# Performance work log

Measured on AMD Instinct MI355X. Metric: run time of the kernel, lower is better.

The kernel has to match this reference:

```python
import jax, jax.numpy as jnp
import numpy as np

B, S, E, H = 2, 2048, 1024, 16
DH = E // H  # 64


def setup_inputs() -> dict:
    key = jax.random.key(0)
    ks = jax.random.split(key, 5)
    scale = 1.0 / np.sqrt(E)
    x = jax.random.normal(ks[0], (B, S, E), dtype=jnp.float32)
    # stacked per-head kqv Linear weights: out = x @ Wkqv[h] + bkqv[h], producing (k, q, v) chunks
    Wkqv = jax.random.normal(ks[1], (H, E, 3 * DH), dtype=jnp.float32) * scale
    bkqv = jax.random.normal(ks[2], (H, 3 * DH), dtype=jnp.float32) * scale
    Wo = jax.random.normal(ks[3], (E, E), dtype=jnp.float32) * scale
    bo = jax.random.normal(ks[4], (E,), dtype=jnp.float32) * scale
    return {"x": x, "Wkqv": Wkqv, "bkqv": bkqv, "Wo": Wo, "bo": bo}


def reference(x, Wkqv, bkqv, Wo, bo):
    b, s, e = x.shape
    h, _, f = Wkqv.shape
    dh = f // 3
    # per-head projection, fused over heads: [b, h, s, 3*dh]
    kqv = jnp.einsum('bse,hef->bhsf', x, Wkqv) + bkqv[None, :, None, :]
    # chunk order in the original is k, q, v
    k, q, v = jnp.split(kqv, 3, axis=-1)
    scores = jnp.einsum('bhqd,bhkd->bhqk', q, k) / jnp.sqrt(jnp.asarray(dh, x.dtype))
    causal = jnp.tril(jnp.ones((s, s), dtype=bool))  # slice of the tril buffer
    scores = jnp.where(causal[None, None], scores, -jnp.inf)
    weights = jax.nn.softmax(scores, axis=-1)
    sa = jnp.einsum('bhqk,bhkd->bhqd', weights, v)
    # concat heads along feature dim (head order preserved)
    sa = sa.transpose(0, 2, 1, 3).reshape(b, s, h * dh)
    return sa @ Wo + bo
```

## Files before the change

### kernel.cpp

```cpp
#include <hip/hip_runtime.h>
#include <hip/hip_bf16.h>

typedef __attribute__((ext_vector_type(8))) short bf16x8;
typedef __attribute__((ext_vector_type(4))) float f32x4;
typedef __attribute__((ext_vector_type(2))) unsigned u32x2;
typedef __attribute__((ext_vector_type(4))) unsigned u32x4;
typedef unsigned short u16;

#define NEG_INF (-__builtin_inff())

__device__ __forceinline__ void gload16(const void* g, void* l) {
  __builtin_amdgcn_global_load_lds(
      (const __attribute__((address_space(1))) void*)g,
      (__attribute__((address_space(3))) void*)l, 16, 0, 0);
}

__device__ __forceinline__ u16 f2b(float f) {
  union { float f; unsigned u; } v;
  v.f = f;
  unsigned r = v.u + 0x7fff + ((v.u >> 16) & 1);
  return (u16)(r >> 16);
}

__device__ __forceinline__ unsigned cvt_pk_bf16(float a, float b) {
  unsigned r;
  asm("v_cvt_pk_bf16_f32 %0, %1, %2" : "=v"(r) : "v"(a), "v"(b));
  return r;
}

__global__ __launch_bounds__(256) void prep_kernel(
    const float* __restrict__ x, u16* __restrict__ xb,
    const float* __restrict__ Wkqv, u16* __restrict__ WkqvT,
    const float* __restrict__ Wo, u16* __restrict__ WoT) {
  __shared__ u16 t[32][33];
  const int bid = blockIdx.x;
  const int tid = threadIdx.x;
  if (bid < 4096) {
    const int i = bid * 256 + tid;
    float4 v = ((const float4*)x)[i];
    ushort2 a = {f2b(v.x), f2b(v.y)}, b = {f2b(v.z), f2b(v.w)};
    ((ushort2*)xb)[i * 2] = a;
    ((ushort2*)xb)[i * 2 + 1] = b;
    return;
  }
  const int tx = tid & 31, ty = tid >> 5;
  const float* src;
  u16* dst;
  int R, C, bx_, by;
  if (bid < 7168) {
    const int tt = bid - 4096;
    const int bz = tt / 192, rem = tt % 192;
    by = rem / 6; bx_ = rem % 6; R = 1024; C = 192;
    src = Wkqv + (size_t)bz * R * C;
    dst = WkqvT + (size_t)bz * R * C;
  } else {
    const int tt = bid - 7168;
    by = tt >> 5; bx_ = tt & 31; R = 1024; C = 1024;
    src = Wo; dst = WoT;
  }
  const int c0 = bx_ * 32, r0 = by * 32;
  for (int i = ty; i < 32; i += 8)
    t[i][tx] = f2b(src[(size_t)(r0 + i) * C + c0 + tx]);
  __syncthreads();
  for (int i = ty; i < 32; i += 8)
    dst[(size_t)(c0 + i) * R + r0 + tx] = t[tx][i];
}

__device__ __forceinline__ void gemm_mainloop_128(
    const __hip_bfloat16* __restrict__ A, const __hip_bfloat16* __restrict__ Bt,
    int K, int m0, int n0, f32x4 acc[4][4], char* AsB, char* BsB) {
  const int tid = threadIdx.x;
  const int wave = tid >> 6, lane = tid & 63;
  const int lhi = lane >> 4, llo = lane & 15;
  const int wr = wave >> 1, wc = wave & 1;
  f32x4 z = {0.f, 0.f, 0.f, 0.f};
#pragma unroll
  for (int i = 0; i < 4; i++)
#pragma unroll
    for (int j = 0; j < 4; j++) acc[i][j] = z;

#define GSTAGE(c, kk)                                                          \
  {                                                                            \
    char* AsW = AsB + (c)*8192;                                                \
    char* BsW = BsB + (c)*8192;                                                \
    _Pragma("unroll") for (int i = 0; i < 2; i++) {                            \
      int cb = i * 256 + wave * 64;                                            \
      int cq = cb + lane;                                                      \
      gload16(A + ((size_t)(m0 + (cq >> 2)) * K + (kk) + (cq & 3) * 8),        \
              AsW + cb * 16);                                                  \
      gload16(Bt + ((size_t)(n0 + (cq >> 2)) * K + (kk) + (cq & 3) * 8),       \
              BsW + cb * 16);                                                  \
    }                                                                          \
  }

  GSTAGE(0, 0);
  int cur = 0;
  const int nk = K >> 5;
  for (int t = 0; t < nk; t++) {
    if (t + 1 < nk) {
      GSTAGE(cur ^ 1, (t + 1) * 32);
      asm volatile("s_waitcnt vmcnt(4)" ::: "memory");
    } else {
      asm volatile("s_waitcnt vmcnt(0)" ::: "memory");
    }
    __builtin_amdgcn_s_barrier();
    __builtin_amdgcn_sched_barrier(0);

    const char* Ar = AsB + cur * 8192;
    const char* Br = BsB + cur * 8192;
    bf16x8 a[4], b[4];
#pragma unroll
    for (int m4 = 0; m4 < 4; m4++)
      a[m4] = *(const bf16x8*)(Ar + (wr * 64 + m4 * 16 + llo) * 64 + lhi * 16);
#pragma unroll
    for (int n4 = 0; n4 < 4; n4++)
      b[n4] = *(const bf16x8*)(Br + (wc * 64 + n4 * 16 + llo) * 64 + lhi * 16);
#pragma unroll
    for (int m4 = 0; m4 < 4; m4++)
#pragma unroll
      for (int n4 = 0; n4 < 4; n4++)
        acc[m4][n4] =
            __builtin_amdgcn_mfma_f32_16x16x32_bf16(a[m4], b[n4], acc[m4][n4], 0, 0, 0);
    __builtin_amdgcn_sched_barrier(0);
    __builtin_amdgcn_s_barrier();
    cur ^= 1;
  }
#undef GSTAGE
}

__device__ __forceinline__ void gemm_mainloop_64x128(
    const __hip_bfloat16* __restrict__ A, const __hip_bfloat16* __restrict__ Bt,
    int K, int m0, int n0, f32x4 acc[2][4], char* AsB, char* BsB) {
  const int tid = threadIdx.x;
  const int wave = tid >> 6, lane = tid & 63;
  const int lhi = lane >> 4, llo = lane & 15;
  const int wr = wave >> 1, wc = wave & 1;
  f32x4 z = {0.f, 0.f, 0.f, 0.f};
#pragma unroll
  for (int i = 0; i < 2; i++)
#pragma unroll
    for (int j = 0; j < 4; j++) acc[i][j] = z;

#define GSTAGE64(c, kk)                                                        \
  {                                                                            \
    char* AsW = AsB + (c)*4096;                                                \
    char* BsW = BsB + (c)*8192;                                                \
    gload16(A + ((size_t)(m0 + (tid >> 2)) * K + (kk) + (tid & 3) * 8),        \
            AsW + (wave * 64) * 16);                                           \
    _Pragma("unroll") for (int i = 0; i < 2; i++) {                            \
      int cb = i * 256 + wave * 64;                                            \
      int cq = cb + lane;                                                      \
      gload16(Bt + ((size_t)(n0 + (cq >> 2)) * K + (kk) + (cq & 3) * 8),       \
              BsW + cb * 16);                                                  \
    }                                                                          \
  }

  GSTAGE64(0, 0);
  int cur = 0;
  const int nk = K >> 5;
  for (int t = 0; t < nk; t++) {
    if (t + 1 < nk) {
      GSTAGE64(cur ^ 1, (t + 1) * 32);
      asm volatile("s_waitcnt vmcnt(3)" ::: "memory");
    } else {
      asm volatile("s_waitcnt vmcnt(0)" ::: "memory");
    }
    __builtin_amdgcn_s_barrier();
    __builtin_amdgcn_sched_barrier(0);

    const char* Ar = AsB + cur * 4096;
    const char* Br = BsB + cur * 8192;
    bf16x8 a[2], b[4];
#pragma unroll
    for (int m2 = 0; m2 < 2; m2++)
      a[m2] = *(const bf16x8*)(Ar + (wr * 32 + m2 * 16 + llo) * 64 + lhi * 16);
#pragma unroll
    for (int n4 = 0; n4 < 4; n4++)
      b[n4] = *(const bf16x8*)(Br + (wc * 64 + n4 * 16 + llo) * 64 + lhi * 16);
#pragma unroll
    for (int m2 = 0; m2 < 2; m2++)
#pragma unroll
      for (int n4 = 0; n4 < 4; n4++)
        acc[m2][n4] =
            __builtin_amdgcn_mfma_f32_16x16x32_bf16(a[m2], b[n4], acc[m2][n4], 0, 0, 0);
    __builtin_amdgcn_sched_barrier(0);
    __builtin_amdgcn_s_barrier();
    cur ^= 1;
  }
#undef GSTAGE64
}

__global__ __launch_bounds__(256) void kqv_gemm(
    const __hip_bfloat16* __restrict__ x, const __hip_bfloat16* __restrict__ WT,
    const float* __restrict__ bkqv, __hip_bfloat16* __restrict__ Qb,
    __hip_bfloat16* __restrict__ Kb, __hip_bfloat16* __restrict__ Vt) {
  __shared__ __align__(16) char As[16384];
  __shared__ __align__(16) char Bs[16384];
  const int m0 = blockIdx.y * 128, n0 = blockIdx.x * 128;
  f32x4 acc[4][4];
  gemm_mainloop_128(x, WT, 1024, m0, n0, acc, As, Bs);

  const int tid = threadIdx.x, wave = tid >> 6, lane = tid & 63;
  const int lhi = lane >> 4, llo = lane & 15;
  const int wr = wave >> 1, wc = wave & 1;
#pragma unroll
  for (int m4 = 0; m4 < 4; m4++)
#pragma unroll
    for (int n4 = 0; n4 < 4; n4++)
#pragma unroll
      for (int r = 0; r < 4; r++) {
        int mg = m0 + wr * 64 + m4 * 16 + lhi * 4 + r;
        int ng = n0 + wc * 64 + n4 * 16 + llo;
        int b = mg >> 11, s = mg & 2047;
        int h = ng / 192, f = ng % 192;
        float v = acc[m4][n4][r] + bkqv[h * 192 + f];
        int chunk = f >> 6, d = f & 63;
        size_t bh = (size_t)(b * 16 + h);
        if (chunk == 0)
          Kb[(bh * 2048 + s) * 64 + d] = __float2bfloat16(v);
        else if (chunk == 1)
          Qb[(bh * 2048 + s) * 64 + d] = __float2bfloat16(v * 0.180336880f);
        else
          Vt[(bh * 64 + d) * 2048 + s] = __float2bfloat16(v);
      }
}

__device__ __forceinline__ void softmax_pack(
    f32x4* s, bool masked, int k0, int qg, int lhi4,
    float& m_s, float& l_s, f32x4* o, bf16x8& ap0, bf16x8& ap1) {
  if (masked) {
#pragma unroll
    for (int jj = 0; jj < 4; jj++)
#pragma unroll
      for (int r = 0; r < 4; r++)
        if (k0 + jj * 16 + lhi4 + r > qg) s[jj][r] = NEG_INF;
  }
  float pmax = s[0][0];
#pragma unroll
  for (int jj = 0; jj < 4; jj++)
#pragma unroll
    for (int r = 0; r < 4; r++) pmax = fmaxf(pmax, s[jj][r]);
  {
    union { float f; unsigned u; } pu;
    pu.f = pmax;
    u32x2 sp = __builtin_amdgcn_permlane32_swap(pu.u, pu.u, false, false);
    float m1 = fmaxf(__uint_as_float(sp.x), __uint_as_float(sp.y));
    union { float f; unsigned u; } mu;
    mu.f = m1;
    u32x2 tp = __builtin_amdgcn_permlane16_swap(mu.u, mu.u, false, false);
    pmax = fmaxf(__uint_as_float(tp.x), __uint_as_float(tp.y));
  }
  if (!__all(pmax - m_s <= 5.0f)) {
    const float mn = fmaxf(m_s, pmax);
    const float sc = __builtin_exp2f(m_s - mn);
    m_s = mn;
    l_s *= sc;
#pragma unroll
    for (int r = 0; r < 4; r++) {
      const float scr = __shfl(sc, lhi4 + r);
#pragma unroll
      for (int n4 = 0; n4 < 4; n4++) o[n4][r] *= scr;
    }
  }
  unsigned pk[4][2];
  float ps = 0.f;
#pragma unroll
  for (int jj = 0; jj < 4; jj++) {
    float p0 = __builtin_exp2f(s[jj][0] - m_s);
    float p1 = __builtin_exp2f(s[jj][1] - m_s);
    float p2 = __builtin_exp2f(s[jj][2] - m_s);
    float p3 = __builtin_exp2f(s[jj][3] - m_s);
    ps += (p0 + p1) + (p2 + p3);
    pk[jj][0] = cvt_pk_bf16(p0, p1);
    pk[jj][1] = cvt_pk_bf16(p2, p3);
  }
  l_s += ps;

  u32x4 a0w, a1w;
#pragma unroll
  for (int u = 0; u < 2; u++) {
    u32x2 sp = __builtin_amdgcn_permlane32_swap(pk[0][u], pk[1][u], false, false);
    u32x2 tp = __builtin_amdgcn_permlane16_swap(sp.x, sp.y, false, false);
    a0w[u] = tp.x;
    a0w[u + 2] = tp.y;
  }
#pragma unroll
  for (int u = 0; u < 2; u++) {
    u32x2 sp = __builtin_amdgcn_permlane32_swap(pk[2][u], pk[3][u], false, false);
    u32x2 tp = __builtin_amdgcn_permlane16_swap(sp.x, sp.y, false, false);
    a1w[u] = tp.x;
    a1w[u + 2] = tp.y;
  }
  ap0 = __builtin_bit_cast(bf16x8, a0w);
  ap1 = __builtin_bit_cast(bf16x8, a1w);
}

__global__ __launch_bounds__(256) void attn_kernel(
    const __hip_bfloat16* __restrict__ Qb, const __hip_bfloat16* __restrict__ Kb,
    const __hip_bfloat16* __restrict__ Vt, __hip_bfloat16* __restrict__ SA) {
  __shared__ __align__(16) char lds[32768];
  const int orig = blockIdx.x;
  const int bh = (orig & 7) * 4 + ((orig >> 3) & 3);
  const int qblk = 15 - (orig >> 5);
  const int nt = 2 * qblk + 2;
  const int b = bh >> 4, h = bh & 15;
  const int tid = threadIdx.x, wave = tid >> 6, lane = tid & 63;
  const int lhi = lane >> 4, llo = lane & 15;
  const int lhi4 = lhi * 4;
  const int wbase = qblk * 128 + wave * 32;

  const __hip_bfloat16* qp =
      Qb + ((size_t)bh * 2048 + wbase + llo) * 64 + lhi * 8;
  bf16x8 qA0 = *(const bf16x8*)qp, qA1 = *(const bf16x8*)(qp + 32);
  bf16x8 qB0 = *(const bf16x8*)(qp + 16 * 64), qB1 = *(const bf16x8*)(qp + 16 * 64 + 32);

  const char* Kg = (const char*)(Kb + (size_t)bh * 2048 * 64);
  const char* Vg = (const char*)(Vt + (size_t)bh * 64 * 2048);

  f32x4 z = {0.f, 0.f, 0.f, 0.f};
  f32x4 o0[4], o1[4];
  float m0 = NEG_INF, l0 = 0.f, m1 = NEG_INF, l1 = 0.f;
#pragma unroll
  for (int i = 0; i < 4; i++) { o0[i] = z; o1[i] = z; }
  const int qg_0 = wbase + llo, qg_1 = wbase + 16 + llo;

#define STAGE(c, k0)                                                          \
  {                                                                           \
    char* KsW = lds + (c)*8192;                                               \
    char* VsW = lds + 16384 + (c)*8192;                                       \
    _Pragma("unroll") for (int i = 0; i < 2; i++) {                           \
      int ch = i * 256 + tid;                                                 \
      int soff = (ch * 16) ^ (((ch >> 3) & 7) << 4);                          \
      gload16(Kg + (size_t)(k0)*128 + soff, KsW + (i * 256 + wave * 64) * 16);\
      int dd = ch >> 3, c8 = ch & 7;                                          \
      int boff = (c8 * 16) ^ ((dd & 7) << 4);                                 \
      gload16(Vg + (size_t)dd * 4096 + (size_t)(k0)*2 + boff,                 \
              VsW + (i * 256 + wave * 64) * 16);                              \
    }                                                                         \
  }

  STAGE(0, 0);
  int cur = 0;

  for (int T = 0; T < nt; T++) {
    if (T + 1 < nt) {
      STAGE(cur ^ 1, (T + 1) * 64);
      asm volatile("s_waitcnt vmcnt(4)" ::: "memory");
    } else {
      asm volatile("s_waitcnt vmcnt(0)" ::: "memory");
    }
    __builtin_amdgcn_s_barrier();
    __builtin_amdgcn_sched_barrier(0);

    const int k0 = T * 64;
    if (k0 <= wbase + 31) {
      const bool act0 = (k0 <= wbase + 15);
      const bool msk0 = (k0 + 63 > wbase);
      const bool msk1 = (k0 + 63 > wbase + 16);
      const char* KsB = lds + cur * 8192;
      const char* VsB = lds + 16384 + cur * 8192;

      f32x4 s[4] = {z, z, z, z}, t[4] = {z, z, z, z};
#pragma unroll
      for (int jj = 0; jj < 4; jj++) {
        const int row = jj * 16 + llo;
        const int rx = (llo & 7) << 4;
        bf16x8 bk0 = *(const bf16x8*)(KsB + ((row * 128 + lhi * 16) ^ rx));
        bf16x8 bk1 = *(const bf16x8*)(KsB + ((row * 128 + 64 + lhi * 16) ^ rx));
        __builtin_amdgcn_s_setprio(1);
        if (act0) {
          s[jj] = __builtin_amdgcn_mfma_f32_16x16x32_bf16(bk0, qA0, s[jj], 0, 0, 0);
          s[jj] = __builtin_amdgcn_mfma_f32_16x16x32_bf16(bk1, qA1, s[jj], 0, 0, 0);
        }
        t[jj] = __builtin_amdgcn_mfma_f32_16x16x32_bf16(bk0, qB0, t[jj], 0, 0, 0);
        t[jj] = __builtin_amdgcn_mfma_f32_16x16x32_bf16(bk1, qB1, t[jj], 0, 0, 0);
        __builtin_amdgcn_s_setprio(0);
      }

      bf16x8 ap0_0, ap1_0, ap0_1, ap1_1;
      if (act0) softmax_pack(s, msk0, k0, qg_0, lhi4, m0, l0, o0, ap0_0, ap1_0);
      softmax_pack(t, msk1, k0, qg_1, lhi4, m1, l1, o1, ap0_1, ap1_1);

#pragma unroll
      for (int n4 = 0; n4 < 4; n4++) {
        const int d = n4 * 16 + llo;
        const int dx = (d & 7) << 4;
        bf16x8 bv0 = *(const bf16x8*)(VsB + ((d * 128 + lhi * 16) ^ dx));
        bf16x8 bv1 = *(const bf16x8*)(VsB + ((d * 128 + 64 + lhi * 16) ^ dx));
        __builtin_amdgcn_s_setprio(1);
        if (act0) {
          o0[n4] = __builtin_amdgcn_mfma_f32_16x16x32_bf16(ap0_0, bv0, o0[n4], 0, 0, 0);
          o0[n4] = __builtin_amdgcn_mfma_f32_16x16x32_bf16(ap1_0, bv1, o0[n4], 0, 0, 0);
        }
        o1[n4] = __builtin_amdgcn_mfma_f32_16x16x32_bf16(ap0_1, bv0, o1[n4], 0, 0, 0);
        o1[n4] = __builtin_amdgcn_mfma_f32_16x16x32_bf16(ap1_1, bv1, o1[n4], 0, 0, 0);
        __builtin_amdgcn_s_setprio(0);
      }
    }
    __builtin_amdgcn_sched_barrier(0);
    __builtin_amdgcn_s_barrier();
    cur ^= 1;
  }

#pragma unroll
  for (int c = 0; c < 2; c++) {
    float l_s = c ? l1 : l0;
    f32x4* o = c ? o1 : o0;
    const int qg0 = wbase + 16 * c + lhi4;
    union { float f; unsigned u; } lu;
    lu.f = l_s;
    u32x2 sp = __builtin_amdgcn_permlane32_swap(lu.u, lu.u, false, false);
    float ls1 = __uint_as_float(sp.x) + __uint_as_float(sp.y);
    union { float f; unsigned u; } l2u;
    l2u.f = ls1;
    u32x2 tp = __builtin_amdgcn_permlane16_swap(l2u.u, l2u.u, false, false);
    const float l = __uint_as_float(tp.x) + __uint_as_float(tp.y);
    const float inv = 1.f / l;
#pragma unroll
    for (int r = 0; r < 4; r++) {
      const float invr = __shfl(inv, lhi4 + r);
      const size_t ob = ((size_t)b * 2048 + qg0 + r) * 1024 + h * 64;
#pragma unroll
      for (int n4 = 0; n4 < 4; n4++)
        SA[ob + n4 * 16 + llo] = __float2bfloat16(o[n4][r] * invr);
    }
  }
#undef STAGE
}

__global__ __launch_bounds__(256) void out_gemm(
    const __hip_bfloat16* __restrict__ SA, const __hip_bfloat16* __restrict__ WoT,
    const float* __restrict__ bo, float* __restrict__ out) {
  __shared__ __align__(16) char As[8192];
  __shared__ __align__(16) char Bs[16384];
  const int m0 = blockIdx.y * 64, n0 = blockIdx.x * 128;
  f32x4 acc[2][4];
  gemm_mainloop_64x128(SA, WoT, 1024, m0, n0, acc, As, Bs);

  const int tid = threadIdx.x, wave = tid >> 6, lane = tid & 63;
  const int lhi = lane >> 4, llo = lane & 15;
  const int wr = wave >> 1, wc = wave & 1;
#pragma unroll
  for (int m2 = 0; m2 < 2; m2++)
#pragma unroll
    for (int n4 = 0; n4 < 4; n4++)
#pragma unroll
      for (int r = 0; r < 4; r++) {
        int mg = m0 + wr * 32 + m2 * 16 + lhi * 4 + r;
        int ng = n0 + wc * 64 + n4 * 16 + llo;
        out[(size_t)mg * 1024 + ng] = acc[m2][n4][r] + bo[ng];
      }
}

extern "C" void kernel_launch(void* const* d_in, const int* in_sizes, int n_in,
                              void* d_out, int out_size, void* d_ws, size_t ws_size,
                              hipStream_t stream) {
  const float* x = (const float*)d_in[0];
  const float* Wkqv = (const float*)d_in[1];
  const float* bkqv = (const float*)d_in[2];
  const float* Wo = (const float*)d_in[3];
  const float* bo = (const float*)d_in[4];
  float* out = (float*)d_out;

  char* w = (char*)d_ws;
  __hip_bfloat16* WkqvT = (__hip_bfloat16*)(w);
  __hip_bfloat16* WoT = (__hip_bfloat16*)(w + 6291456);
  __hip_bfloat16* Qb = (__hip_bfloat16*)(w + 8388608);
  __hip_bfloat16* Kb = (__hip_bfloat16*)(w + 16777216);
  __hip_bfloat16* Vt = (__hip_bfloat16*)(w + 25165824);
  __hip_bfloat16* SAb = (__hip_bfloat16*)(w + 33554432);
  __hip_bfloat16* xb = (__hip_bfloat16*)(w + 41943040);

  prep_kernel<<<8192, 256, 0, stream>>>(x, (u16*)xb, Wkqv, (u16*)WkqvT,
                                        Wo, (u16*)WoT);
  kqv_gemm<<<dim3(24, 32), 256, 0, stream>>>(xb, WkqvT, bkqv, Qb, Kb, Vt);
  attn_kernel<<<512, 256, 0, stream>>>(Qb, Kb, Vt, SAb);
  out_gemm<<<dim3(8, 64), 256, 0, stream>>>(SAb, WoT, bo, out);
}
```

Baseline: 137.4 us.

## Halve attention block size to 64 queries and stage V transpose through LDS

The attention kernel now runs 1024 blocks of 128 threads, each covering a 64-query tile. This removes the per-wave inactive and skip branches, and only the final diagonal tile is masked. The goal is better load balance and more resident blocks under the causal mask, at the cost of fetching K/V tiles twice as often per query. Separately, the KQV GEMM epilogue writes the V chunk into an LDS transpose buffer and then stores it to Vt with coalesced 16-byte writes, replacing strided 2-byte scatter stores. The price is an extra barrier and LDS traffic.

```diff
diff --git a/kernel.cpp b/kernel.cpp
--- a/kernel.cpp
+++ b/kernel.cpp
@@ -194,35 +194,52 @@
     const __hip_bfloat16* __restrict__ x, const __hip_bfloat16* __restrict__ WT,
     const float* __restrict__ bkqv, __hip_bfloat16* __restrict__ Qb,
     __hip_bfloat16* __restrict__ Kb, __hip_bfloat16* __restrict__ Vt) {
-  __shared__ __align__(16) char As[16384];
-  __shared__ __align__(16) char Bs[16384];
+  __shared__ __align__(16) char ldsbuf[34816];
   const int m0 = blockIdx.y * 128, n0 = blockIdx.x * 128;
   f32x4 acc[4][4];
-  gemm_mainloop_128(x, WT, 1024, m0, n0, acc, As, Bs);
+  gemm_mainloop_128(x, WT, 1024, m0, n0, acc, ldsbuf, ldsbuf + 16384);
 
   const int tid = threadIdx.x, wave = tid >> 6, lane = tid & 63;
   const int lhi = lane >> 4, llo = lane & 15;
   const int wr = wave >> 1, wc = wave & 1;
+  u16* Vsw = (u16*)ldsbuf;
 #pragma unroll
   for (int m4 = 0; m4 < 4; m4++)
 #pragma unroll
     for (int n4 = 0; n4 < 4; n4++)
 #pragma unroll
       for (int r = 0; r < 4; r++) {
-        int mg = m0 + wr * 64 + m4 * 16 + lhi * 4 + r;
-        int ng = n0 + wc * 64 + n4 * 16 + llo;
+        int sp = wr * 64 + m4 * 16 + lhi * 4 + r;
+        int row = wc * 64 + n4 * 16 + llo;
+        int mg = m0 + sp;
+        int ng = n0 + row;
         int b = mg >> 11, s = mg & 2047;
         int h = ng / 192, f = ng % 192;
         float v = acc[m4][n4][r] + bkqv[h * 192 + f];
-        int chunk = f >> 6, d = f & 63;
+        int d = f & 63;
         size_t bh = (size_t)(b * 16 + h);
-        if (chunk == 0)
+        if (f < 64)
           Kb[(bh * 2048 + s) * 64 + d] = __float2bfloat16(v);
-        else if (chunk == 1)
+        else if (f < 128)
           Qb[(bh * 2048 + s) * 64 + d] = __float2bfloat16(v * 0.180336880f);
         else
-          Vt[(bh * 64 + d) * 2048 + s] = __float2bfloat16(v);
+          Vsw[row * 136 + sp] = f2b(v);
       }
+  __syncthreads();
+#pragma unroll
+  for (int it = 0; it < 8; it++) {
+    int task = it * 256 + tid;
+    int row = task >> 4, c = task & 15;
+    int ng = n0 + row, f = ng % 192;
+    if (f >= 128) {
+      int h = ng / 192, d = f - 128;
+      int mg0 = m0 + c * 8;
+      int b = mg0 >> 11, s = mg0 & 2047;
+      size_t bh = (size_t)(b * 16 + h);
+      u32x4 w = *(const u32x4*)&Vsw[row * 136 + c * 8];
+      *(u32x4*)((u16*)Vt + (size_t)(bh * 64 + d) * 2048 + s) = w;
+    }
+  }
 }
 
 __device__ __forceinline__ void softmax_pack(
@@ -295,24 +312,25 @@
   ap1 = __builtin_bit_cast(bf16x8, a1w);
 }
 
-__global__ __launch_bounds__(256) void attn_kernel(
+__global__ __launch_bounds__(128) void attn_kernel(
     const __hip_bfloat16* __restrict__ Qb, const __hip_bfloat16* __restrict__ Kb,
     const __hip_bfloat16* __restrict__ Vt, __hip_bfloat16* __restrict__ SA) {
   __shared__ __align__(16) char lds[32768];
   const int orig = blockIdx.x;
   const int bh = (orig & 7) * 4 + ((orig >> 3) & 3);
-  const int qblk = 15 - (orig >> 5);
-  const int nt = 2 * qblk + 2;
+  const int qt = 31 - (orig >> 5);
+  const int nt = qt + 1;
   const int b = bh >> 4, h = bh & 15;
   const int tid = threadIdx.x, wave = tid >> 6, lane = tid & 63;
   const int lhi = lane >> 4, llo = lane & 15;
   const int lhi4 = lhi * 4;
-  const int wbase = qblk * 128 + wave * 32;
+  const int wbase = qt * 64 + wave * 32;
 
   const __hip_bfloat16* qp =
       Qb + ((size_t)bh * 2048 + wbase + llo) * 64 + lhi * 8;
   bf16x8 qA0 = *(const bf16x8*)qp, qA1 = *(const bf16x8*)(qp + 32);
-  bf16x8 qB0 = *(const bf16x8*)(qp + 16 * 64), qB1 = *(const bf16x8*)(qp + 16 * 64 + 32);
+  bf16x8 qB0 = *(const bf16x8*)(qp + 16 * 64);
+  bf16x8 qB1 = *(const bf16x8*)(qp + 16 * 64 + 32);
 
   const char* Kg = (const char*)(Kb + (size_t)bh * 2048 * 64);
   const char* Vg = (const char*)(Vt + (size_t)bh * 64 * 2048);
@@ -328,14 +346,14 @@
   {                                                                           \
     char* KsW = lds + (c)*8192;                                               \
     char* VsW = lds + 16384 + (c)*8192;                                       \
-    _Pragma("unroll") for (int i = 0; i < 2; i++) {                           \
-      int ch = i * 256 + tid;                                                 \
+    _Pragma("unroll") for (int i = 0; i < 4; i++) {                           \
+      int ch = i * 128 + tid;                                                 \
       int soff = (ch * 16) ^ (((ch >> 3) & 7) << 4);                          \
-      gload16(Kg + (size_t)(k0)*128 + soff, KsW + (i * 256 + wave * 64) * 16);\
+      gload16(Kg + (size_t)(k0)*128 + soff, KsW + (i * 128 + wave * 64) * 16);\
       int dd = ch >> 3, c8 = ch & 7;                                          \
       int boff = (c8 * 16) ^ ((dd & 7) << 4);                                 \
       gload16(Vg + (size_t)dd * 4096 + (size_t)(k0)*2 + boff,                 \
-              VsW + (i * 256 + wave * 64) * 16);                              \
+              VsW + (i * 128 + wave * 64) * 16);                              \
     }                                                                         \
   }
 
@@ -345,7 +363,7 @@
   for (int T = 0; T < nt; T++) {
     if (T + 1 < nt) {
       STAGE(cur ^ 1, (T + 1) * 64);
-      asm volatile("s_waitcnt vmcnt(4)" ::: "memory");
+      asm volatile("s_waitcnt vmcnt(8)" ::: "memory");
     } else {
       asm volatile("s_waitcnt vmcnt(0)" ::: "memory");
     }
@@ -353,49 +371,41 @@
     __builtin_amdgcn_sched_barrier(0);
 
     const int k0 = T * 64;
-    if (k0 <= wbase + 31) {
-      const bool act0 = (k0 <= wbase + 15);
-      const bool msk0 = (k0 + 63 > wbase);
-      const bool msk1 = (k0 + 63 > wbase + 16);
-      const char* KsB = lds + cur * 8192;
-      const char* VsB = lds + 16384 + cur * 8192;
-
-      f32x4 s[4] = {z, z, z, z}, t[4] = {z, z, z, z};
-#pragma unroll
-      for (int jj = 0; jj < 4; jj++) {
-        const int row = jj * 16 + llo;
-        const int rx = (llo & 7) << 4;
-        bf16x8 bk0 = *(const bf16x8*)(KsB + ((row * 128 + lhi * 16) ^ rx));
-        bf16x8 bk1 = *(const bf16x8*)(KsB + ((row * 128 + 64 + lhi * 16) ^ rx));
-        __builtin_amdgcn_s_setprio(1);
-        if (act0) {
-          s[jj] = __builtin_amdgcn_mfma_f32_16x16x32_bf16(bk0, qA0, s[jj], 0, 0, 0);
-          s[jj] = __builtin_amdgcn_mfma_f32_16x16x32_bf16(bk1, qA1, s[jj], 0, 0, 0);
-        }
-        t[jj] = __builtin_amdgcn_mfma_f32_16x16x32_bf16(bk0, qB0, t[jj], 0, 0, 0);
-        t[jj] = __builtin_amdgcn_mfma_f32_16x16x32_bf16(bk1, qB1, t[jj], 0, 0, 0);
-        __builtin_amdgcn_s_setprio(0);
-      }
-
-      bf16x8 ap0_0, ap1_0, ap0_1, ap1_1;
-      if (act0) softmax_pack(s, msk0, k0, qg_0, lhi4, m0, l0, o0, ap0_0, ap1_0);
-      softmax_pack(t, msk1, k0, qg_1, lhi4, m1, l1, o1, ap0_1, ap1_1);
-
-#pragma unroll
-      for (int n4 = 0; n4 < 4; n4++) {
-        const int d = n4 * 16 + llo;
-        const int dx = (d & 7) << 4;
-        bf16x8 bv0 = *(const bf16x8*)(VsB + ((d * 128 + lhi * 16) ^ dx));
-        bf16x8 bv1 = *(const bf16x8*)(VsB + ((d * 128 + 64 + lhi * 16) ^ dx));
-        __builtin_amdgcn_s_setprio(1);
-        if (act0) {
-          o0[n4] = __builtin_amdgcn_mfma_f32_16x16x32_bf16(ap0_0, bv0, o0[n4], 0, 0, 0);
-          o0[n4] = __builtin_amdgcn_mfma_f32_16x16x32_bf16(ap1_0, bv1, o0[n4], 0, 0, 0);
-        }
-        o1[n4] = __builtin_amdgcn_mfma_f32_16x16x32_bf16(ap0_1, bv0, o1[n4], 0, 0, 0);
-        o1[n4] = __builtin_amdgcn_mfma_f32_16x16x32_bf16(ap1_1, bv1, o1[n4], 0, 0, 0);
-        __builtin_amdgcn_s_setprio(0);
-      }
+    const bool masked = (T == nt - 1);
+    const char* KsB = lds + cur * 8192;
+    const char* VsB = lds + 16384 + cur * 8192;
+
+    f32x4 s[4] = {z, z, z, z}, t[4] = {z, z, z, z};
+#pragma unroll
+    for (int jj = 0; jj < 4; jj++) {
+      const int row = jj * 16 + llo;
+      const int rx = (row & 7) << 4;
+      bf16x8 bk0 = *(const bf16x8*)(KsB + ((row * 128 + lhi * 16) ^ rx));
+      bf16x8 bk1 = *(const bf16x8*)(KsB + ((row * 128 + 64 + lhi * 16) ^ rx));
+      __builtin_amdgcn_s_setprio(1);
+      s[jj] = __builtin_amdgcn_mfma_f32_16x16x32_bf16(bk0, qA0, s[jj], 0, 0, 0);
+      s[jj] = __builtin_amdgcn_mfma_f32_16x16x32_bf16(bk1, qA1, s[jj], 0, 0, 0);
+      t[jj] = __builtin_amdgcn_mfma_f32_16x16x32_bf16(bk0, qB0, t[jj], 0, 0, 0);
+      t[jj] = __builtin_amdgcn_mfma_f32_16x16x32_bf16(bk1, qB1, t[jj], 0, 0, 0);
+      __builtin_amdgcn_s_setprio(0);
+    }
+
+    bf16x8 ap0_0, ap1_0, ap0_1, ap1_1;
+    softmax_pack(s, masked, k0, qg_0, lhi4, m0, l0, o0, ap0_0, ap1_0);
+    softmax_pack(t, masked, k0, qg_1, lhi4, m1, l1, o1, ap0_1, ap1_1);
+
+#pragma unroll
+    for (int n4 = 0; n4 < 4; n4++) {
+      const int d = n4 * 16 + llo;
+      const int dx = (d & 7) << 4;
+      bf16x8 bv0 = *(const bf16x8*)(VsB + ((d * 128 + lhi * 16) ^ dx));
+      bf16x8 bv1 = *(const bf16x8*)(VsB + ((d * 128 + 64 + lhi * 16) ^ dx));
+      __builtin_amdgcn_s_setprio(1);
+      o0[n4] = __builtin_amdgcn_mfma_f32_16x16x32_bf16(ap0_0, bv0, o0[n4], 0, 0, 0);
+      o0[n4] = __builtin_amdgcn_mfma_f32_16x16x32_bf16(ap1_0, bv1, o0[n4], 0, 0, 0);
+      o1[n4] = __builtin_amdgcn_mfma_f32_16x16x32_bf16(ap0_1, bv0, o1[n4], 0, 0, 0);
+      o1[n4] = __builtin_amdgcn_mfma_f32_16x16x32_bf16(ap1_1, bv1, o1[n4], 0, 0, 0);
+      __builtin_amdgcn_s_setprio(0);
     }
     __builtin_amdgcn_sched_barrier(0);
     __builtin_amdgcn_s_barrier();
@@ -474,6 +484,6 @@
   prep_kernel<<<8192, 256, 0, stream>>>(x, (u16*)xb, Wkqv, (u16*)WkqvT,
                                         Wo, (u16*)WoT);
   kqv_gemm<<<dim3(24, 32), 256, 0, stream>>>(xb, WkqvT, bkqv, Qb, Kb, Vt);
-  attn_kernel<<<512, 256, 0, stream>>>(Qb, Kb, Vt, SAb);
+  attn_kernel<<<1024, 128, 0, stream>>>(Qb, Kb, Vt, SAb);
   out_gemm<<<dim3(8, 64), 256, 0, stream>>>(SAb, WoT, bo, out);
 }
```

After: 136.6 us. No clear change (-0.6%).
